# Kernel optimization log

Hardware: AMD Instinct MI355X
Metric: run time of the kernel (lower is better)

Reference implementation:

```python
import jax, jax.numpy as jnp
import numpy as np


def setup_inputs() -> dict:
    key = jax.random.key(0)
    k1, k2, k3 = jax.random.split(key, 3)
    x = jax.random.normal(k1, (8, 3, 256, 256), dtype=jnp.float32)
    conv_w = jax.random.normal(k2, (64, 3), dtype=jnp.float32)  # 1x1 conv weight [O, C]
    w = jax.random.normal(k3, (64, 8), dtype=jnp.float32)       # per-channel LBP weights
    return {"x": x, "conv_w": conv_w, "w": w}


def _heaviside(d):
    # torch.heaviside(d, 0.): 1 where d > 0, else 0 (including d == 0)
    return jnp.where(d > 0, jnp.ones((), d.dtype), jnp.zeros((), d.dtype))


def reference(x, conv_w, w):
    # 1x1 conv, no bias: [N,C,H,W] x [O,C] -> [N,O,H,W]
    y = jnp.einsum('nchw,oc->nohw', x, conv_w)
    c = y[:, :, 1:-1, 1:-1]  # center, [N,O,H-2,W-2]
    # 8 neighbor shifts in the original order
    shifts = [
        y[:, :, 0:-2, 0:-2], y[:, :, 0:-2, 1:-1], y[:, :, 0:-2, 2:],
        y[:, :, 1:-1, 0:-2], y[:, :, 2:, 0:-2], y[:, :, 2:, 1:-1],
        y[:, :, 2:, 2:],    y[:, :, 1:-1, 2:],
    ]
    act = jnp.stack([_heaviside(c - s) for s in shifts], axis=2)  # [N,O,8,H-2,W-2]
    # weighted reduction over the 8 directions with exp(w)
    x_cat = jnp.einsum('nolhw,ol->nohw', act, jnp.exp(w))
    padded = jnp.pad(x_cat, ((0, 0), (0, 0), (1, 1), (1, 1)))  # ZeroPad2d(1)
    # res=True: concat raw input along channels -> [N, 3+O, H, W]
    return jnp.concatenate([x, padded], axis=1)
```

## Files before the change

kernel.cpp:

```cpp
#include <hip/hip_runtime.h>


__global__ __launch_bounds__(256) void copy_x_kernel(
    const float* __restrict__ x, float* __restrict__ out)
{
    const int n   = blockIdx.z;
    const int c   = blockIdx.y;
    const int tid = threadIdx.x;
    const int h   = blockIdx.x * 4 + (tid >> 6);
    const int wq  = (tid & 63) * 4;
    const float4 v = *(const float4*)(x + ((((size_t)n * 3 + c) * 256 + h) * 256 + wq));
    *(float4*)(out + ((((size_t)n * 67 + c) * 256 + h) * 256 + wq)) = v;
}

__global__ __launch_bounds__(256) void lbp_kernel(
    const float* __restrict__ x,
    const float* __restrict__ conv_w,
    const float* __restrict__ w,
    float* __restrict__ out)
{
#pragma clang fp contract(off)
    const int n    = blockIdx.z;
    const int o    = blockIdx.y;
    const int h0   = blockIdx.x * 8;
    const int tid  = threadIdx.x;
    const int lane = tid & 63;
    const int wv   = tid >> 6;

    __shared__ float ylds[10][256];
    __shared__ float ews[8];

    if (tid < 8) ews[tid] = expf(w[o * 8 + tid]);

    const float cw0 = conv_w[o * 3 + 0];
    const float cw1 = conv_w[o * 3 + 1];
    const float cw2 = conv_w[o * 3 + 2];
    const float* xn = x + (size_t)n * 3 * 256 * 256;
    const int col = lane * 4;

    #pragma unroll
    for (int p = 0; p < 3; ++p) {
        const int i = p * 4 + wv;
        if (i < 10) {
            int row = h0 - 1 + i;
            row = row < 0 ? 0 : (row > 255 ? 255 : row);
            const float4 a = *(const float4*)(xn + (0 * 256 + row) * 256 + col);
            const float4 b = *(const float4*)(xn + (1 * 256 + row) * 256 + col);
            const float4 c = *(const float4*)(xn + (2 * 256 + row) * 256 + col);
            float4 yv;
            yv.x = a.x * cw0 + b.x * cw1 + c.x * cw2;
            yv.y = a.y * cw0 + b.y * cw1 + c.y * cw2;
            yv.z = a.z * cw0 + b.z * cw1 + c.z * cw2;
            yv.w = a.w * cw0 + b.w * cw1 + c.w * cw2;
            *(float4*)&ylds[i][col] = yv;
        }
    }
    __syncthreads();

    const float e0 = ews[0], e1 = ews[1], e2 = ews[2], e3 = ews[3];
    const float e4 = ews[4], e5 = ews[5], e6 = ews[6], e7 = ews[7];

    float Y[4][6];
    #pragma unroll
    for (int r = 0; r < 4; ++r) {
        const float4 v = *(const float4*)&ylds[2 * wv + r][col];
        Y[r][1] = v.x; Y[r][2] = v.y; Y[r][3] = v.z; Y[r][4] = v.w;
        Y[r][0] = __shfl_up(v.w, 1);
        Y[r][5] = __shfl_down(v.x, 1);
    }

    float* outp = out + ((((size_t)n * 67 + 3 + o) * 256 + h0) * 256);

    #pragma unroll
    for (int jr = 0; jr < 2; ++jr) {
        const int hrow = h0 + 2 * wv + jr;
        float res[4];
        if (hrow == 0 || hrow == 255) {
            res[0] = res[1] = res[2] = res[3] = 0.f;
        } else {
            const float* up = Y[jr];
            const float* mid = Y[jr + 1];
            const float* dn = Y[jr + 2];
            #pragma unroll
            for (int j = 0; j < 4; ++j) {
                const int cidx = col + j;
                if ((cidx == 0) | (cidx == 255)) { res[j] = 0.f; continue; }
                const float c = mid[j + 1];
                float acc;
                acc  = (c > up [j    ]) ? e0 : 0.f;
                acc += (c > up [j + 1]) ? e1 : 0.f;
                acc += (c > up [j + 2]) ? e2 : 0.f;
                acc += (c > mid[j    ]) ? e3 : 0.f;
                acc += (c > dn [j    ]) ? e4 : 0.f;
                acc += (c > dn [j + 1]) ? e5 : 0.f;
                acc += (c > dn [j + 2]) ? e6 : 0.f;
                acc += (c > mid[j + 2]) ? e7 : 0.f;
                res[j] = acc;
            }
        }
        *(float4*)(outp + (size_t)(2 * wv + jr) * 256 + col) =
            make_float4(res[0], res[1], res[2], res[3]);
    }
}

extern "C" void kernel_launch(void* const* d_in, const int* in_sizes, int n_in,
                              void* d_out, int out_size, void* d_ws, size_t ws_size,
                              hipStream_t stream) {
    const float* x      = (const float*)d_in[0];
    const float* conv_w = (const float*)d_in[1];
    const float* w      = (const float*)d_in[2];
    float* out          = (float*)d_out;

    hipLaunchKernelGGL(copy_x_kernel, dim3(64, 3, 8), dim3(256), 0, stream, x, out);
    hipLaunchKernelGGL(lbp_kernel, dim3(32, 64, 8), dim3(256), 0, stream,
                       x, conv_w, w, out);
}
```

Before: 158.5 us.

## Fuse input copy into LBP kernel and process eight output channels per block

Merges the separate copy kernel into the LBP kernel: blocks with og==0 write the raw input rows to the output while staging them. Each block now loads a 6-row, 3-channel input tile into shared memory once and loops over 8 output channels, recomputing the 1x1 conv per channel. This cuts redundant global reads of x and one kernel launch. In exchange, each block handles fewer rows and adds two barriers per channel iteration.

```diff
diff --git a/kernel.cpp b/kernel.cpp
--- a/kernel.cpp
+++ b/kernel.cpp
@@ -1,19 +1,7 @@
 #include <hip/hip_runtime.h>
 
 
-__global__ __launch_bounds__(256) void copy_x_kernel(
-    const float* __restrict__ x, float* __restrict__ out)
-{
-    const int n   = blockIdx.z;
-    const int c   = blockIdx.y;
-    const int tid = threadIdx.x;
-    const int h   = blockIdx.x * 4 + (tid >> 6);
-    const int wq  = (tid & 63) * 4;
-    const float4 v = *(const float4*)(x + ((((size_t)n * 3 + c) * 256 + h) * 256 + wq));
-    *(float4*)(out + ((((size_t)n * 67 + c) * 256 + h) * 256 + wq)) = v;
-}
-
-__global__ __launch_bounds__(256) void lbp_kernel(
+__global__ __launch_bounds__(256) void lbp_all(
     const float* __restrict__ x,
     const float* __restrict__ conv_w,
     const float* __restrict__ w,
@@ -21,85 +9,101 @@
 {
 #pragma clang fp contract(off)
     const int n    = blockIdx.z;
-    const int o    = blockIdx.y;
-    const int h0   = blockIdx.x * 8;
+    const int og   = blockIdx.y;
+    const int h0   = blockIdx.x * 4;
     const int tid  = threadIdx.x;
     const int lane = tid & 63;
     const int wv   = tid >> 6;
+    const int col  = lane * 4;
 
-    __shared__ float ylds[10][256];
-    __shared__ float ews[8];
+    __shared__ float xs[6][3][256];
+    __shared__ float ys[6][256];
+    __shared__ float ews[64];
 
-    if (tid < 8) ews[tid] = expf(w[o * 8 + tid]);
+    if (tid < 64) ews[tid] = expf(w[og * 64 + tid]);
 
-    const float cw0 = conv_w[o * 3 + 0];
-    const float cw1 = conv_w[o * 3 + 1];
-    const float cw2 = conv_w[o * 3 + 2];
     const float* xn = x + (size_t)n * 3 * 256 * 256;
-    const int col = lane * 4;
 
     #pragma unroll
-    for (int p = 0; p < 3; ++p) {
-        const int i = p * 4 + wv;
-        if (i < 10) {
-            int row = h0 - 1 + i;
+    for (int p = 0; p < 5; ++p) {
+        const int u = wv + 4 * p;
+        if (u < 18) {
+            const int r  = u / 3;
+            const int ch = u % 3;
+            int row = h0 - 1 + r;
             row = row < 0 ? 0 : (row > 255 ? 255 : row);
-            const float4 a = *(const float4*)(xn + (0 * 256 + row) * 256 + col);
-            const float4 b = *(const float4*)(xn + (1 * 256 + row) * 256 + col);
-            const float4 c = *(const float4*)(xn + (2 * 256 + row) * 256 + col);
-            float4 yv;
-            yv.x = a.x * cw0 + b.x * cw1 + c.x * cw2;
-            yv.y = a.y * cw0 + b.y * cw1 + c.y * cw2;
-            yv.z = a.z * cw0 + b.z * cw1 + c.z * cw2;
-            yv.w = a.w * cw0 + b.w * cw1 + c.w * cw2;
-            *(float4*)&ylds[i][col] = yv;
+            const float4 v = *(const float4*)(xn + ((ch * 256 + row) * 256 + col));
+            *(float4*)&xs[r][ch][col] = v;
+            if (og == 0 && r >= 1 && r <= 4) {
+                *(float4*)(out + ((((size_t)n * 67 + ch) * 256 + (h0 + r - 1)) * 256 + col)) = v;
+            }
         }
     }
     __syncthreads();
 
-    const float e0 = ews[0], e1 = ews[1], e2 = ews[2], e3 = ews[3];
-    const float e4 = ews[4], e5 = ews[5], e6 = ews[6], e7 = ews[7];
+    for (int oi = 0; oi < 8; ++oi) {
+        const int o = og * 8 + oi;
+        const float cw0 = conv_w[o * 3 + 0];
+        const float cw1 = conv_w[o * 3 + 1];
+        const float cw2 = conv_w[o * 3 + 2];
 
-    float Y[4][6];
-    #pragma unroll
-    for (int r = 0; r < 4; ++r) {
-        const float4 v = *(const float4*)&ylds[2 * wv + r][col];
-        Y[r][1] = v.x; Y[r][2] = v.y; Y[r][3] = v.z; Y[r][4] = v.w;
-        Y[r][0] = __shfl_up(v.w, 1);
-        Y[r][5] = __shfl_down(v.x, 1);
-    }
+        #pragma unroll
+        for (int p = 0; p < 2; ++p) {
+            const int r = wv + 4 * p;
+            if (r < 6) {
+                const float4 a = *(const float4*)&xs[r][0][col];
+                const float4 b = *(const float4*)&xs[r][1][col];
+                const float4 c = *(const float4*)&xs[r][2][col];
+                float4 yv;
+                yv.x = a.x * cw0 + b.x * cw1 + c.x * cw2;
+                yv.y = a.y * cw0 + b.y * cw1 + c.y * cw2;
+                yv.z = a.z * cw0 + b.z * cw1 + c.z * cw2;
+                yv.w = a.w * cw0 + b.w * cw1 + c.w * cw2;
+                *(float4*)&ys[r][col] = yv;
+            }
+        }
+        __syncthreads();
 
-    float* outp = out + ((((size_t)n * 67 + 3 + o) * 256 + h0) * 256);
+        float Y[3][6];
+        #pragma unroll
+        for (int r = 0; r < 3; ++r) {
+            const float4 v = *(const float4*)&ys[wv + r][col];
+            Y[r][1] = v.x; Y[r][2] = v.y; Y[r][3] = v.z; Y[r][4] = v.w;
+            Y[r][0] = __shfl_up(v.w, 1);
+            Y[r][5] = __shfl_down(v.x, 1);
+        }
 
-    #pragma unroll
-    for (int jr = 0; jr < 2; ++jr) {
-        const int hrow = h0 + 2 * wv + jr;
+        const float e0 = ews[oi * 8 + 0], e1 = ews[oi * 8 + 1];
+        const float e2 = ews[oi * 8 + 2], e3 = ews[oi * 8 + 3];
+        const float e4 = ews[oi * 8 + 4], e5 = ews[oi * 8 + 5];
+        const float e6 = ews[oi * 8 + 6], e7 = ews[oi * 8 + 7];
+
+        const int hrow = h0 + wv;
         float res[4];
         if (hrow == 0 || hrow == 255) {
             res[0] = res[1] = res[2] = res[3] = 0.f;
         } else {
-            const float* up = Y[jr];
-            const float* mid = Y[jr + 1];
-            const float* dn = Y[jr + 2];
             #pragma unroll
             for (int j = 0; j < 4; ++j) {
                 const int cidx = col + j;
                 if ((cidx == 0) | (cidx == 255)) { res[j] = 0.f; continue; }
-                const float c = mid[j + 1];
+                const float c = Y[1][j + 1];
                 float acc;
-                acc  = (c > up [j    ]) ? e0 : 0.f;
-                acc += (c > up [j + 1]) ? e1 : 0.f;
-                acc += (c > up [j + 2]) ? e2 : 0.f;
-                acc += (c > mid[j    ]) ? e3 : 0.f;
-                acc += (c > dn [j    ]) ? e4 : 0.f;
-                acc += (c > dn [j + 1]) ? e5 : 0.f;
-                acc += (c > dn [j + 2]) ? e6 : 0.f;
-                acc += (c > mid[j + 2]) ? e7 : 0.f;
+                acc  = (c > Y[0][j    ]) ? e0 : 0.f;
+                acc += (c > Y[0][j + 1]) ? e1 : 0.f;
+                acc += (c > Y[0][j + 2]) ? e2 : 0.f;
+                acc += (c > Y[1][j    ]) ? e3 : 0.f;
+                acc += (c > Y[2][j    ]) ? e4 : 0.f;
+                acc += (c > Y[2][j + 1]) ? e5 : 0.f;
+                acc += (c > Y[2][j + 2]) ? e6 : 0.f;
+                acc += (c > Y[1][j + 2]) ? e7 : 0.f;
                 res[j] = acc;
             }
         }
-        *(float4*)(outp + (size_t)(2 * wv + jr) * 256 + col) =
+        *(float4*)(out + ((((size_t)n * 67 + 3 + o) * 256 + hrow) * 256 + col)) =
             make_float4(res[0], res[1], res[2], res[3]);
+
+        __syncthreads();
     }
 }
 
@@ -111,7 +115,7 @@
     const float* w      = (const float*)d_in[2];
     float* out          = (float*)d_out;
 
-    hipLaunchKernelGGL(copy_x_kernel, dim3(64, 3, 8), dim3(256), 0, stream, x, out);
-    hipLaunchKernelGGL(lbp_kernel, dim3(32, 64, 8), dim3(256), 0, stream,
-                       x, conv_w, w, out);
+    dim3 grid(64, 8, 8);
+    dim3 block(256);
+    hipLaunchKernelGGL(lbp_all, grid, block, 0, stream, x, conv_w, w, out);
 }
```

New measurement: 163.2 us. 3.0% more time.
